# Kernel optimization log

Hardware: AMD Instinct MI355X
Metric: run time of the kernel (lower is better)

Reference implementation:

```python
import jax, jax.numpy as jnp
import numpy as np
from jax import lax

B, S, E, H = 4, 1024, 512, 8
D = E // H


def setup_inputs() -> dict:
    key = jax.random.key(0)
    k1, k2, k3 = jax.random.split(key, 3)
    source = jax.random.normal(k1, (B, S, E), dtype=jnp.float32)
    target = jax.random.normal(k2, (B, S, E), dtype=jnp.float32)
    # orthogonal-initialized positional encoder [1, H, 1, D]; random rows are a fine stand-in
    enc = jax.random.normal(k3, (1, H, 1, D), dtype=jnp.float32)
    enc = enc / jnp.linalg.norm(enc, axis=-1, keepdims=True)
    return {
        "source": source,
        "target": target,
        "encoder": enc,
        "alpha": jnp.float32(1.0),
        "beta": jnp.float32(1.0),
        "gamma": jnp.float32(2.0),
    }


def _split_heads(x):
    b, s, e = x.shape
    return x.reshape(b, s, H, e // H).transpose(0, 2, 1, 3)  # [B,H,S,D]


def reference(source, target, encoder, alpha, beta, gamma):
    q = _split_heads(source)  # [B,H,S,D]
    k = _split_heads(target)  # [B,H,S,D]
    pe = encoder[0, :, 0, :]  # [H,D]

    # --- grammar (time) attention: sequential tanh recurrence over t ---
    def step(cc, k_t):
        # cc, k_t: [B,H,D]
        cc = jnp.tanh(cc * pe)
        out = jnp.einsum('bhsd,bhd->bhs', q, cc)  # [B,H,S]
        return k_t * cc, out  # decay_rate = 0.0

    cc0 = k[:, :, 0, :]                      # initial cumulative context
    k_ts = jnp.moveaxis(k, 2, 0)             # [S,B,H,D]
    _, outs = lax.scan(step, cc0, k_ts)      # outs: [S,B,H,S]
    grammar = jnp.moveaxis(outs, 0, 3) / jnp.sqrt(jnp.float32(D))  # [B,H,S,S]
    grammar = jax.nn.softmax(grammar, axis=-1)

    # --- semantic attention ---
    semantic = jnp.einsum('bhsd,bhtd->bhst', q, k) / 100.0  # [B,H,S,S]

    w = jax.nn.softmax((alpha * semantic + beta * grammar) / gamma, axis=-1)

    # merge_heads: [B,H,S,S] -> [B,S,H*S]
    wm = w.transpose(0, 2, 1, 3).reshape(B, S, H * S)
    # output: wm^T @ target -> [B, H*S, E]
    return jnp.matmul(wm.transpose(0, 2, 1), target)
```

## Files before the change

kernel.cpp:

```cpp
#include <hip/hip_runtime.h>
#include <hip/hip_bf16.h>
#include <stdint.h>

#define S_LEN 1024
#define E_DIM 512
#define H_NUM 8
#define D_DIM 64
#define B_NUM 4
#define BH_NUM 32

using s16x8 = __attribute__((ext_vector_type(8))) short;
using f32x4 = __attribute__((ext_vector_type(4))) float;
using us4   = __attribute__((ext_vector_type(4))) unsigned short;

static __device__ __forceinline__ unsigned short f2bf(float f) {
  __hip_bfloat16 h = __float2bfloat16(f);
  return __builtin_bit_cast(unsigned short, h);
}
static __device__ __forceinline__ float bf2f(unsigned short u) {
  return __bfloat162float(__builtin_bit_cast(__hip_bfloat16, u));
}

#define NB_RECUR 8
#define NB_PACK  2048
#define NB_TR    512

__global__ __launch_bounds__(256) void k_prep(const float* __restrict__ src,
                                              const float* __restrict__ tgt,
                                              const float* __restrict__ enc,
                                              __hip_bfloat16* __restrict__ qb,
                                              __hip_bfloat16* __restrict__ kb,
                                              __hip_bfloat16* __restrict__ cb,
                                              __hip_bfloat16* __restrict__ tT) {
  __shared__ float tile[64][65];
  const int bid = blockIdx.x;
  const int tid = threadIdx.x;

  if (bid < NB_RECUR) {
    int g = bid * 256 + tid;
    int d = g & 63;
    int bh = g >> 6;
    int h = bh & 7;
    int b = bh >> 3;
    float pe = enc[h * D_DIM + d];
    float pe2 = 2.0f * pe;
    const float* tp = tgt + (size_t)b * S_LEN * E_DIM + h * D_DIM + d;
    __hip_bfloat16* cp = cb + (size_t)bh * S_LEN * D_DIM + d;

    constexpr int CH = 32;
    float bufA[CH], bufB[CH];
#pragma unroll
    for (int i = 0; i < CH; ++i) bufA[i] = tp[(size_t)i * E_DIM];
    float cc = bufA[0];

#pragma unroll 1
    for (int ch = 0; ch < S_LEN / CH; ch += 2) {
      if (ch + 1 < S_LEN / CH) {
#pragma unroll
        for (int i = 0; i < CH; ++i)
          bufB[i] = tp[(size_t)((ch + 1) * CH + i) * E_DIM];
      }
#pragma unroll
      for (int i = 0; i < CH; ++i) {
        float m = cc * pe2;
        float e = __expf(-fabsf(m));
        float th = __builtin_copysignf((1.0f - e) * __builtin_amdgcn_rcpf(1.0f + e), m);
        cp[(size_t)(ch * CH + i) * D_DIM] = __float2bfloat16(th);
        cc = bufA[i] * th;
      }
      if (ch + 2 < S_LEN / CH) {
#pragma unroll
        for (int i = 0; i < CH; ++i)
          bufA[i] = tp[(size_t)((ch + 2) * CH + i) * E_DIM];
      }
#pragma unroll
      for (int i = 0; i < CH; ++i) {
        float m = cc * pe2;
        float e = __expf(-fabsf(m));
        float th = __builtin_copysignf((1.0f - e) * __builtin_amdgcn_rcpf(1.0f + e), m);
        cp[(size_t)((ch + 1) * CH + i) * D_DIM] = __float2bfloat16(th);
        cc = bufB[i] * th;
      }
    }
  } else if (bid < NB_RECUR + NB_PACK) {
    size_t i4 = ((size_t)(bid - NB_RECUR) * 256 + tid) * 4;
    float4 s4 = *reinterpret_cast<const float4*>(src + i4);
    float4 t4 = *reinterpret_cast<const float4*>(tgt + i4);
    int e = (int)(i4 & 511);
    size_t bs = i4 >> 9;
    int s = (int)(bs & 1023);
    int b = (int)(bs >> 10);
    int h = e >> 6, d = e & 63;
    size_t o = (((size_t)(b * H_NUM + h) * S_LEN) + s) * D_DIM + d;
    us4 qv = {f2bf(s4.x), f2bf(s4.y), f2bf(s4.z), f2bf(s4.w)};
    us4 kv = {f2bf(t4.x), f2bf(t4.y), f2bf(t4.z), f2bf(t4.w)};
    *reinterpret_cast<us4*>(qb + o) = qv;
    *reinterpret_cast<us4*>(kb + o) = kv;
  } else {
    int lb = bid - (NB_RECUR + NB_PACK);
    int sx = lb & 15, ey = (lb >> 4) & 7, b = lb >> 7;
    int e0 = ey * 64, s0 = sx * 64;
    int tx = tid & 63, ty = tid >> 6;
    const float* p = tgt + ((size_t)b * S_LEN + s0) * E_DIM + e0;
#pragma unroll
    for (int r = ty; r < 64; r += 4) tile[r][tx] = p[(size_t)r * E_DIM + tx];
    __syncthreads();
    __hip_bfloat16* q = tT + ((size_t)b * E_DIM + e0) * S_LEN + s0;
#pragma unroll
    for (int r = ty; r < 64; r += 4) q[(size_t)r * S_LEN + tx] = __float2bfloat16(tile[tx][r]);
  }
}

__global__ __launch_bounds__(256) void k_weights(const __hip_bfloat16* __restrict__ qb,
                                                 const __hip_bfloat16* __restrict__ kb,
                                                 const __hip_bfloat16* __restrict__ cb,
                                                 __hip_bfloat16* __restrict__ wt,
                                                 const float* __restrict__ pal,
                                                 const float* __restrict__ pbe,
                                                 const float* __restrict__ pga) {
  __shared__ float red0[4][16];
  __shared__ float red1[4][16];

  const int tid = threadIdx.x;
  const int wave = tid >> 6, lane = tid & 63;
  const int quad = lane >> 4, col = lane & 15;

  const int g = blockIdx.x;
  const int xcd = g & 7;
  const int r = g >> 3;
  const int bh = xcd * 4 + (r >> 6);
  const int s0 = (r & 63) * 16;

  const float alpha = pal[0], beta = pbe[0];
  const float inv_gamma = 1.0f / pga[0];
  const float sa = alpha * 0.01f * inv_gamma;
  const float sb = beta * inv_gamma;

  const __hip_bfloat16* qrow = qb + ((size_t)bh * S_LEN + s0 + col) * D_DIM;
  s16x8 a0 = *reinterpret_cast<const s16x8*>(qrow + quad * 8);
  s16x8 a1 = *reinterpret_cast<const s16x8*>(qrow + 32 + quad * 8);

  const int t_base = wave * 256;
  uint32_t stg[16][2];
  float    stk[16][4];

  const __hip_bfloat16* cbh = cb + ((size_t)bh * S_LEN + t_base + col) * D_DIM;
  const __hip_bfloat16* kbh = kb + ((size_t)bh * S_LEN + t_base + col) * D_DIM;
  float lg[4] = {0.f, 0.f, 0.f, 0.f};
#pragma unroll
  for (int it = 0; it < 16; ++it) {
    const __hip_bfloat16* crow = cbh + (size_t)it * 16 * D_DIM;
    const __hip_bfloat16* krow = kbh + (size_t)it * 16 * D_DIM;
    s16x8 cb0 = *reinterpret_cast<const s16x8*>(crow + quad * 8);
    s16x8 cb1 = *reinterpret_cast<const s16x8*>(crow + 32 + quad * 8);
    s16x8 kb0 = *reinterpret_cast<const s16x8*>(krow + quad * 8);
    s16x8 kb1 = *reinterpret_cast<const s16x8*>(krow + 32 + quad * 8);
    f32x4 dg = {0.f, 0.f, 0.f, 0.f};
    dg = __builtin_amdgcn_mfma_f32_16x16x32_bf16(a0, cb0, dg, 0, 0, 0);
    dg = __builtin_amdgcn_mfma_f32_16x16x32_bf16(a1, cb1, dg, 0, 0, 0);
    f32x4 dk = {0.f, 0.f, 0.f, 0.f};
    dk = __builtin_amdgcn_mfma_f32_16x16x32_bf16(a0, kb0, dk, 0, 0, 0);
    dk = __builtin_amdgcn_mfma_f32_16x16x32_bf16(a1, kb1, dk, 0, 0, 0);
    uint32_t p0 = 0, p1 = 0;
#pragma unroll
    for (int i = 0; i < 4; ++i) {
      float gv = __expf(dg[i] * 0.125f);
      unsigned short u = f2bf(gv);
      lg[i] += bf2f(u);
      if (i < 2) p0 |= (uint32_t)u << (16 * i);
      else       p1 |= (uint32_t)u << (16 * (i - 2));
      stk[it][i] = dk[i];
    }
    stg[it][0] = p0;
    stg[it][1] = p1;
  }
#pragma unroll
  for (int m = 1; m < 16; m <<= 1) {
#pragma unroll
    for (int i = 0; i < 4; ++i) lg[i] += __shfl_xor(lg[i], m);
  }
  if (col == 0) {
#pragma unroll
    for (int i = 0; i < 4; ++i) red0[wave][quad * 4 + i] = lg[i];
  }
  __syncthreads();
  float ilg[4];
#pragma unroll
  for (int i = 0; i < 4; ++i) {
    int rr = quad * 4 + i;
    ilg[i] = 1.0f / (red0[0][rr] + red0[1][rr] + red0[2][rr] + red0[3][rr]);
  }

  float lw[4] = {0.f, 0.f, 0.f, 0.f};
#pragma unroll
  for (int it = 0; it < 16; ++it) {
#pragma unroll
    for (int i = 0; i < 4; ++i) {
      unsigned short u = (unsigned short)((i < 2 ? stg[it][0] >> (16 * i)
                                                 : stg[it][1] >> (16 * (i - 2))) & 0xffffu);
      float gv = bf2f(u) * ilg[i];
      float z = sa * stk[it][i] + sb * gv;
      float wv = __expf(z);
      stk[it][i] = wv;
      lw[i] += wv;
    }
  }
#pragma unroll
  for (int m = 1; m < 16; m <<= 1) {
#pragma unroll
    for (int i = 0; i < 4; ++i) lw[i] += __shfl_xor(lw[i], m);
  }
  if (col == 0) {
#pragma unroll
    for (int i = 0; i < 4; ++i) red1[wave][quad * 4 + i] = lw[i];
  }
  __syncthreads();
  float ilw[4];
#pragma unroll
  for (int i = 0; i < 4; ++i) {
    int rr = quad * 4 + i;
    ilw[i] = 1.0f / (red1[0][rr] + red1[1][rr] + red1[2][rr] + red1[3][rr]);
  }

  __hip_bfloat16* wrow = wt + ((size_t)bh * S_LEN + t_base + col) * S_LEN + s0 + quad * 4;
#pragma unroll
  for (int it = 0; it < 16; ++it) {
    us4 o;
#pragma unroll
    for (int i = 0; i < 4; ++i) o[i] = f2bf(stk[it][i] * ilw[i]);
    *reinterpret_cast<us4*>(wrow + (size_t)it * 16 * S_LEN) = o;
  }
}

typedef const __attribute__((address_space(1))) uint32_t gas_uint;
typedef __attribute__((address_space(3))) uint32_t las_uint;

__global__ __launch_bounds__(256) void k_outgemm(const __hip_bfloat16* __restrict__ wt,
                                                 const __hip_bfloat16* __restrict__ tT,
                                                 float* __restrict__ out) {
  __shared__ __hip_bfloat16 As[128 * 64];
  __shared__ __hip_bfloat16 Bs[128 * 64];
  const int tid = threadIdx.x;
  const int wave = tid >> 6, lane = tid & 63;
  const int quad = lane >> 4, col = lane & 15;

  const int g = blockIdx.x;
  const int xcd = g & 7;
  const int local = g >> 3;
  const int strip = xcd * 32 + (local >> 2);
  const int ntile = local & 3;
  const int bh = strip >> 3;
  const int mt = strip & 7;
  const int b = bh >> 3;
  const int m0 = mt * 128;
  const int n0 = ntile * 128;

  const __hip_bfloat16* Ag = wt + (size_t)bh * S_LEN * S_LEN;
  const __hip_bfloat16* Bg = tT + (size_t)b * E_DIM * S_LEN;
  const int mw = (wave >> 1) * 64, nw = (wave & 1) * 64;
  const int lrow = lane >> 3;
  const int lcol = (lane & 7) * 8;

  f32x4 acc[4][4];
#pragma unroll
  for (int i = 0; i < 4; ++i)
#pragma unroll
    for (int j = 0; j < 4; ++j) acc[i][j] = (f32x4){0.f, 0.f, 0.f, 0.f};

  for (int kt = 0; kt < 16; ++kt) {
    const int k0 = kt * 64;
    __syncthreads();
#pragma unroll
    for (int j = 0; j < 4; ++j) {
      int row = j * 32 + wave * 8 + lrow;
      const __hip_bfloat16* gp = Ag + (size_t)(m0 + row) * S_LEN + k0 + lcol;
      __builtin_amdgcn_global_load_lds((gas_uint*)gp,
                                       (las_uint*)(As + (j * 32 + wave * 8) * 64),
                                       16, 0, 0);
    }
#pragma unroll
    for (int j = 0; j < 4; ++j) {
      int row = j * 32 + wave * 8 + lrow;
      const __hip_bfloat16* gp = Bg + (size_t)(n0 + row) * S_LEN + k0 + lcol;
      __builtin_amdgcn_global_load_lds((gas_uint*)gp,
                                       (las_uint*)(Bs + (j * 32 + wave * 8) * 64),
                                       16, 0, 0);
    }
    __syncthreads();
#pragma unroll
    for (int ks = 0; ks < 2; ++ks) {
      s16x8 af[4], bf[4];
#pragma unroll
      for (int i = 0; i < 4; ++i)
        af[i] = *reinterpret_cast<const s16x8*>(As + (mw + i * 16 + col) * 64 + ks * 32 + quad * 8);
#pragma unroll
      for (int i = 0; i < 4; ++i)
        bf[i] = *reinterpret_cast<const s16x8*>(Bs + (nw + i * 16 + col) * 64 + ks * 32 + quad * 8);
#pragma unroll
      for (int mi = 0; mi < 4; ++mi)
#pragma unroll
        for (int ni = 0; ni < 4; ++ni)
          acc[mi][ni] = __builtin_amdgcn_mfma_f32_16x16x32_bf16(af[mi], bf[ni], acc[mi][ni], 0, 0, 0);
    }
  }

#pragma unroll
  for (int mi = 0; mi < 4; ++mi)
#pragma unroll
    for (int ni = 0; ni < 4; ++ni)
#pragma unroll
      for (int i = 0; i < 4; ++i) {
        int m = m0 + mw + mi * 16 + quad * 4 + i;
        int n = n0 + nw + ni * 16 + col;
        out[((size_t)bh * S_LEN + m) * E_DIM + n] = acc[mi][ni][i];
      }
}

extern "C" void kernel_launch(void* const* d_in, const int* in_sizes, int n_in,
                              void* d_out, int out_size, void* d_ws, size_t ws_size,
                              hipStream_t stream) {
  (void)in_sizes; (void)n_in; (void)out_size; (void)ws_size;
  const float* src = (const float*)d_in[0];
  const float* tgt = (const float*)d_in[1];
  const float* enc = (const float*)d_in[2];
  const float* pal = (const float*)d_in[3];
  const float* pbe = (const float*)d_in[4];
  const float* pga = (const float*)d_in[5];
  float* out = (float*)d_out;

  char* ws = (char*)d_ws;
  __hip_bfloat16* qb = (__hip_bfloat16*)(ws);
  __hip_bfloat16* kb = (__hip_bfloat16*)(ws + ((size_t)4 << 20));
  __hip_bfloat16* cb = (__hip_bfloat16*)(ws + ((size_t)8 << 20));
  __hip_bfloat16* tT = (__hip_bfloat16*)(ws + ((size_t)12 << 20));
  __hip_bfloat16* wt = (__hip_bfloat16*)(ws + ((size_t)16 << 20));

  k_prep<<<NB_RECUR + NB_PACK + NB_TR, 256, 0, stream>>>(src, tgt, enc, qb, kb, cb, tT);
  k_weights<<<dim3((S_LEN / 16) * BH_NUM), 256, 0, stream>>>(qb, kb, cb, wt, pal, pbe, pga);
  k_outgemm<<<dim3((E_DIM / 128) * (S_LEN / 128) * BH_NUM), 256, 0, stream>>>(wt, tT, out);
}
```

Measured before the change: 245.9 us.

## Share K/C tiles across query rows via double-buffered LDS in weights kernel

The weights kernel now uses 1024-thread blocks covering 64 query rows instead of 16. The C and K key tiles are streamed into LDS with async global_load_lds in double-buffered 256-row chunks, so each key row is fetched from global memory once per 64 queries rather than once per 16. Output stores are staged through a padded LDS tile so each row writes 64 contiguous bf16 values instead of scattered 8-byte pieces. This costs about 128 KB of LDS per block plus extra barriers, which limits occupancy to one block per CU and keeps register pressure high from the held per-thread stg/stk arrays.

Result: slower. 294.6 us (+19.8%).

```diff
diff --git a/kernel.cpp b/kernel.cpp
--- a/kernel.cpp
+++ b/kernel.cpp
@@ -20,6 +20,9 @@
 static __device__ __forceinline__ float bf2f(unsigned short u) {
   return __bfloat162float(__builtin_bit_cast(__hip_bfloat16, u));
 }
+
+typedef const __attribute__((address_space(1))) uint32_t gas_uint;
+typedef __attribute__((address_space(3))) uint32_t las_uint;
 
 #define NB_RECUR 8
 #define NB_PACK  2048
@@ -111,69 +114,103 @@
   }
 }
 
-__global__ __launch_bounds__(256) void k_weights(const __hip_bfloat16* __restrict__ qb,
-                                                 const __hip_bfloat16* __restrict__ kb,
-                                                 const __hip_bfloat16* __restrict__ cb,
-                                                 __hip_bfloat16* __restrict__ wt,
-                                                 const float* __restrict__ pal,
-                                                 const float* __restrict__ pbe,
-                                                 const float* __restrict__ pga) {
-  __shared__ float red0[4][16];
-  __shared__ float red1[4][16];
+#define SW 72
+
+__global__ __launch_bounds__(1024) void k_weights(const __hip_bfloat16* __restrict__ qb,
+                                                  const __hip_bfloat16* __restrict__ kb,
+                                                  const __hip_bfloat16* __restrict__ cb,
+                                                  __hip_bfloat16* __restrict__ wt,
+                                                  const float* __restrict__ pal,
+                                                  const float* __restrict__ pbe,
+                                                  const float* __restrict__ pga) {
+  __shared__ __hip_bfloat16 lbuf[2][2][256 * D_DIM];
+  __shared__ float redg[4][4][16];
+  __shared__ float redw[4][4][16];
 
   const int tid = threadIdx.x;
   const int wave = tid >> 6, lane = tid & 63;
   const int quad = lane >> 4, col = lane & 15;
+  const int sg = wave & 3;
+  const int ts = wave >> 2;
 
   const int g = blockIdx.x;
   const int xcd = g & 7;
   const int r = g >> 3;
-  const int bh = xcd * 4 + (r >> 6);
-  const int s0 = (r & 63) * 16;
+  const int bh = xcd * 4 + (r >> 4);
+  const int s0 = (r & 15) * 64;
 
   const float alpha = pal[0], beta = pbe[0];
   const float inv_gamma = 1.0f / pga[0];
   const float sa = alpha * 0.01f * inv_gamma;
   const float sb = beta * inv_gamma;
 
-  const __hip_bfloat16* qrow = qb + ((size_t)bh * S_LEN + s0 + col) * D_DIM;
+  const __hip_bfloat16* qrow = qb + ((size_t)bh * S_LEN + s0 + sg * 16 + col) * D_DIM;
   s16x8 a0 = *reinterpret_cast<const s16x8*>(qrow + quad * 8);
   s16x8 a1 = *reinterpret_cast<const s16x8*>(qrow + 32 + quad * 8);
 
-  const int t_base = wave * 256;
-  uint32_t stg[16][2];
+  const __hip_bfloat16* cbh = cb + (size_t)bh * S_LEN * D_DIM;
+  const __hip_bfloat16* kbh = kb + (size_t)bh * S_LEN * D_DIM;
+
+  uint32_t stg_[16][2];
   float    stk[16][4];
 
-  const __hip_bfloat16* cbh = cb + ((size_t)bh * S_LEN + t_base + col) * D_DIM;
-  const __hip_bfloat16* kbh = kb + ((size_t)bh * S_LEN + t_base + col) * D_DIM;
+#pragma unroll
+  for (int rr = 0; rr < 2; ++rr) {
+    size_t l = (size_t)rr * 8192 + wave * 512;
+    __builtin_amdgcn_global_load_lds((gas_uint*)(cbh + l + lane * 8),
+                                     (las_uint*)(&lbuf[0][0][l]), 16, 0, 0);
+    __builtin_amdgcn_global_load_lds((gas_uint*)(kbh + l + lane * 8),
+                                     (las_uint*)(&lbuf[0][1][l]), 16, 0, 0);
+  }
+  __syncthreads();
+
   float lg[4] = {0.f, 0.f, 0.f, 0.f};
-#pragma unroll
-  for (int it = 0; it < 16; ++it) {
-    const __hip_bfloat16* crow = cbh + (size_t)it * 16 * D_DIM;
-    const __hip_bfloat16* krow = kbh + (size_t)it * 16 * D_DIM;
-    s16x8 cb0 = *reinterpret_cast<const s16x8*>(crow + quad * 8);
-    s16x8 cb1 = *reinterpret_cast<const s16x8*>(crow + 32 + quad * 8);
-    s16x8 kb0 = *reinterpret_cast<const s16x8*>(krow + quad * 8);
-    s16x8 kb1 = *reinterpret_cast<const s16x8*>(krow + 32 + quad * 8);
-    f32x4 dg = {0.f, 0.f, 0.f, 0.f};
-    dg = __builtin_amdgcn_mfma_f32_16x16x32_bf16(a0, cb0, dg, 0, 0, 0);
-    dg = __builtin_amdgcn_mfma_f32_16x16x32_bf16(a1, cb1, dg, 0, 0, 0);
-    f32x4 dk = {0.f, 0.f, 0.f, 0.f};
-    dk = __builtin_amdgcn_mfma_f32_16x16x32_bf16(a0, kb0, dk, 0, 0, 0);
-    dk = __builtin_amdgcn_mfma_f32_16x16x32_bf16(a1, kb1, dk, 0, 0, 0);
-    uint32_t p0 = 0, p1 = 0;
-#pragma unroll
-    for (int i = 0; i < 4; ++i) {
-      float gv = __expf(dg[i] * 0.125f);
-      unsigned short u = f2bf(gv);
-      lg[i] += bf2f(u);
-      if (i < 2) p0 |= (uint32_t)u << (16 * i);
-      else       p1 |= (uint32_t)u << (16 * (i - 2));
-      stk[it][i] = dk[i];
-    }
-    stg[it][0] = p0;
-    stg[it][1] = p1;
-  }
+#pragma unroll 1
+  for (int c = 0; c < 4; ++c) {
+    const int pb = c & 1;
+    if (c < 3) {
+      const size_t chunk_off = (size_t)(c + 1) * 256 * D_DIM;
+#pragma unroll
+      for (int rr = 0; rr < 2; ++rr) {
+        size_t l = (size_t)rr * 8192 + wave * 512;
+        __builtin_amdgcn_global_load_lds((gas_uint*)(cbh + chunk_off + l + lane * 8),
+                                         (las_uint*)(&lbuf[pb ^ 1][0][l]), 16, 0, 0);
+        __builtin_amdgcn_global_load_lds((gas_uint*)(kbh + chunk_off + l + lane * 8),
+                                         (las_uint*)(&lbuf[pb ^ 1][1][l]), 16, 0, 0);
+      }
+    }
+#pragma unroll
+    for (int itl = 0; itl < 4; ++itl) {
+      const int itg = c * 4 + itl;
+      const int t_l = ts * 64 + itl * 16 + col;
+      const __hip_bfloat16* crow = &lbuf[pb][0][(size_t)t_l * D_DIM];
+      const __hip_bfloat16* krow = &lbuf[pb][1][(size_t)t_l * D_DIM];
+      s16x8 cb0 = *reinterpret_cast<const s16x8*>(crow + quad * 8);
+      s16x8 cb1 = *reinterpret_cast<const s16x8*>(crow + 32 + quad * 8);
+      s16x8 kb0 = *reinterpret_cast<const s16x8*>(krow + quad * 8);
+      s16x8 kb1 = *reinterpret_cast<const s16x8*>(krow + 32 + quad * 8);
+      f32x4 dg = {0.f, 0.f, 0.f, 0.f};
+      dg = __builtin_amdgcn_mfma_f32_16x16x32_bf16(a0, cb0, dg, 0, 0, 0);
+      dg = __builtin_amdgcn_mfma_f32_16x16x32_bf16(a1, cb1, dg, 0, 0, 0);
+      f32x4 dk = {0.f, 0.f, 0.f, 0.f};
+      dk = __builtin_amdgcn_mfma_f32_16x16x32_bf16(a0, kb0, dk, 0, 0, 0);
+      dk = __builtin_amdgcn_mfma_f32_16x16x32_bf16(a1, kb1, dk, 0, 0, 0);
+      uint32_t p0 = 0, p1 = 0;
+#pragma unroll
+      for (int i = 0; i < 4; ++i) {
+        float gv = __expf(dg[i] * 0.125f);
+        unsigned short u = f2bf(gv);
+        lg[i] += bf2f(u);
+        if (i < 2) p0 |= (uint32_t)u << (16 * i);
+        else       p1 |= (uint32_t)u << (16 * (i - 2));
+        stk[itg][i] = dk[i];
+      }
+      stg_[itg][0] = p0;
+      stg_[itg][1] = p1;
+    }
+    __syncthreads();
+  }
+
 #pragma unroll
   for (int m = 1; m < 16; m <<= 1) {
 #pragma unroll
@@ -181,27 +218,27 @@
   }
   if (col == 0) {
 #pragma unroll
-    for (int i = 0; i < 4; ++i) red0[wave][quad * 4 + i] = lg[i];
+    for (int i = 0; i < 4; ++i) redg[ts][sg][quad * 4 + i] = lg[i];
   }
   __syncthreads();
   float ilg[4];
 #pragma unroll
   for (int i = 0; i < 4; ++i) {
     int rr = quad * 4 + i;
-    ilg[i] = 1.0f / (red0[0][rr] + red0[1][rr] + red0[2][rr] + red0[3][rr]);
+    ilg[i] = 1.0f / (redg[0][sg][rr] + redg[1][sg][rr] + redg[2][sg][rr] + redg[3][sg][rr]);
   }
 
   float lw[4] = {0.f, 0.f, 0.f, 0.f};
 #pragma unroll
-  for (int it = 0; it < 16; ++it) {
+  for (int itg = 0; itg < 16; ++itg) {
 #pragma unroll
     for (int i = 0; i < 4; ++i) {
-      unsigned short u = (unsigned short)((i < 2 ? stg[it][0] >> (16 * i)
-                                                 : stg[it][1] >> (16 * (i - 2))) & 0xffffu);
+      unsigned short u = (unsigned short)((i < 2 ? stg_[itg][0] >> (16 * i)
+                                                 : stg_[itg][1] >> (16 * (i - 2))) & 0xffffu);
       float gv = bf2f(u) * ilg[i];
-      float z = sa * stk[it][i] + sb * gv;
+      float z = sa * stk[itg][i] + sb * gv;
       float wv = __expf(z);
-      stk[it][i] = wv;
+      stk[itg][i] = wv;
       lw[i] += wv;
     }
   }
@@ -212,28 +249,38 @@
   }
   if (col == 0) {
 #pragma unroll
-    for (int i = 0; i < 4; ++i) red1[wave][quad * 4 + i] = lw[i];
+    for (int i = 0; i < 4; ++i) redw[ts][sg][quad * 4 + i] = lw[i];
   }
   __syncthreads();
   float ilw[4];
 #pragma unroll
   for (int i = 0; i < 4; ++i) {
     int rr = quad * 4 + i;
-    ilw[i] = 1.0f / (red1[0][rr] + red1[1][rr] + red1[2][rr] + red1[3][rr]);
-  }
-
-  __hip_bfloat16* wrow = wt + ((size_t)bh * S_LEN + t_base + col) * S_LEN + s0 + quad * 4;
-#pragma unroll
-  for (int it = 0; it < 16; ++it) {
-    us4 o;
-#pragma unroll
-    for (int i = 0; i < 4; ++i) o[i] = f2bf(stk[it][i] * ilw[i]);
-    *reinterpret_cast<us4*>(wrow + (size_t)it * 16 * S_LEN) = o;
-  }
-}
-
-typedef const __attribute__((address_space(1))) uint32_t gas_uint;
-typedef __attribute__((address_space(3))) uint32_t las_uint;
+    ilw[i] = 1.0f / (redw[0][sg][rr] + redw[1][sg][rr] + redw[2][sg][rr] + redw[3][sg][rr]);
+  }
+
+  __hip_bfloat16* tb = &lbuf[0][0][0];
+#pragma unroll 1
+  for (int c = 0; c < 4; ++c) {
+    __syncthreads();
+#pragma unroll
+    for (int itl = 0; itl < 4; ++itl) {
+      const int t_l = ts * 64 + itl * 16 + col;
+      us4 o;
+#pragma unroll
+      for (int i = 0; i < 4; ++i) o[i] = f2bf(stk[c * 4 + itl][i] * ilw[i]);
+      *reinterpret_cast<us4*>(&tb[(size_t)t_l * SW + sg * 16 + quad * 4]) = o;
+    }
+    __syncthreads();
+#pragma unroll
+    for (int rr = 0; rr < 4; ++rr) {
+      const int t_l = rr * 64 + (tid >> 4);
+      const int s4 = (tid & 15) * 4;
+      us4 v = *reinterpret_cast<const us4*>(&tb[(size_t)t_l * SW + s4]);
+      *reinterpret_cast<us4*>(wt + ((size_t)bh * S_LEN + c * 256 + t_l) * S_LEN + s0 + s4) = v;
+    }
+  }
+}
 
 __global__ __launch_bounds__(256) void k_outgemm(const __hip_bfloat16* __restrict__ wt,
                                                  const __hip_bfloat16* __restrict__ tT,
@@ -336,6 +383,6 @@
   __hip_bfloat16* wt = (__hip_bfloat16*)(ws + ((size_t)16 << 20));
 
   k_prep<<<NB_RECUR + NB_PACK + NB_TR, 256, 0, stream>>>(src, tgt, enc, qb, kb, cb, tT);
-  k_weights<<<dim3((S_LEN / 16) * BH_NUM), 256, 0, stream>>>(qb, kb, cb, wt, pal, pbe, pga);
+  k_weights<<<dim3(512), 1024, 0, stream>>>(qb, kb, cb, wt, pal, pbe, pga);
   k_outgemm<<<dim3((E_DIM / 128) * (S_LEN / 128) * BH_NUM), 256, 0, stream>>>(wt, tT, out);
 }
```
